# Performance work log

Hardware: AMD Instinct MI355X
Metric: run time of the kernel (lower is better)

## Reference

```python
import jax, jax.numpy as jnp
import numpy as np

B, INP, OUP = 16, 64, 64
T, H, W = 30, 64, 44
KD, KH, KW = 3, 3, 3
M, G = 2, 2
INP_GAP = max(16, INP // 16)          # 16
GROUPS = G * OUP                       # 128 (wn_fc2 groups)
IN_PG = (M * OUP) // GROUPS            # 1  in-channels per group
OUT_PG = (OUP * INP * KD * KH * KW) // GROUPS  # 864 out-channels per group


def setup_inputs() -> dict:
    key = jax.random.key(0)
    ks = jax.random.split(key, 6)
    x = jax.random.normal(ks[0], (B, INP, T, H, W), dtype=jnp.float32)
    # reduce: 1x1x1 conv INP -> INP_GAP (with bias), acts on [B, INP, 1,1,1]
    w_reduce = jax.random.normal(ks[1], (INP_GAP, INP), dtype=jnp.float32) * 0.05
    b_reduce = jax.random.normal(ks[2], (INP_GAP,), dtype=jnp.float32) * 0.05
    # wn_fc1: 1x1x1 conv INP_GAP -> M*OUP (with bias)
    w_fc1 = jax.random.normal(ks[3], (M * OUP, INP_GAP), dtype=jnp.float32) * 0.05
    b_fc1 = jax.random.normal(ks[4], (M * OUP,), dtype=jnp.float32) * 0.05
    # wn_fc2: grouped 1x1x1 conv, no bias: [groups, out_per_group, in_per_group]
    w_fc2 = jax.random.normal(ks[5], (GROUPS, OUT_PG, IN_PG), dtype=jnp.float32) * 0.02
    return {"x": x, "w_reduce": w_reduce, "b_reduce": b_reduce,
            "w_fc1": w_fc1, "b_fc1": b_fc1, "w_fc2": w_fc2}


def reference(x, w_reduce, b_reduce, w_fc1, b_fc1, w_fc2):
    # Global average pool over T,H,W -> [B, INP]; 1x1x1 convs are matmuls.
    x_gap = x.mean(axis=(2, 3, 4))                       # [B, INP]
    g = x_gap @ w_reduce.T + b_reduce                     # [B, INP_GAP]
    h = jax.nn.sigmoid(g @ w_fc1.T + b_fc1)               # [B, M*OUP]
    # Grouped 1x1 conv (groups=GROUPS): group-major channel layout matches
    # torch's conv output ordering, so a plain reshape reproduces .view().
    hg = h.reshape(B, GROUPS, IN_PG)                      # [B, G*OUP, 1]
    wdyn = jnp.einsum('goi,bgi->bgo', w_fc2, hg)          # [B, GROUPS, OUT_PG]
    wdyn = wdyn.reshape(B, OUP, INP, KD, KH, KW)          # per-sample conv weights

    # Per-sample conv3d (groups=1), stride 1, padding 1 on D,H,W.
    def conv_one(xi, wi):
        # xi: [INP, T, H, W], wi: [OUP, INP, KD, KH, KW]
        return jax.lax.conv_general_dilated(
            xi[None], wi, window_strides=(1, 1, 1),
            padding=[(1, 1), (1, 1), (1, 1)],
            dimension_numbers=('NCDHW', 'OIDHW', 'NCDHW'))[0]

    return jax.vmap(conv_one)(x, wdyn)                    # [B, OUP, T, H, W]
```

## Files before the change

kernel.cpp:

```cpp
#include <hip/hip_runtime.h>
#include <hip/hip_bf16.h>
#include <stdint.h>

#define B_ 16
#define T_ 30
#define H_ 64
#define W_ 44
#define HW_ (H_*W_)
#define THW_ (T_*HW_)

#define HP_ 66
#define WP_ 46
#define PPLANE_ (HP_*WP_)
#define PPOS_ (T_*PPLANE_)

#define SZ2 4
#define SY2 10
#define SX2 18
#define NS2 (SZ2*SY2*SX2)

#define SWZ(v) (((v) >> 1) & 3)

typedef __bf16 bf16x8 __attribute__((ext_vector_type(8)));
typedef float f32x4 __attribute__((ext_vector_type(4)));

static __device__ __forceinline__ short f2bf(float f) {
    __hip_bfloat16 h = __float2bfloat16(f);
    union { __hip_bfloat16 b; short s; } u; u.b = h; return u.s;
}

static __device__ __forceinline__ void gload_lds16(const short* g, short* l) {
    __builtin_amdgcn_global_load_lds((const __attribute__((address_space(1))) void*)g,
                                     (__attribute__((address_space(3))) void*)l, 16, 0, 0);
}

__global__ __launch_bounds__(256) void transpose_kernel(const float* __restrict__ x,
                                                        short* __restrict__ xt,
                                                        float* __restrict__ gap) {
    __shared__ short lb[64*52];
    __shared__ float gsum[64];
    int blk = blockIdx.x;
    int b = blk / (T_*HP_);
    int r = blk - b*(T_*HP_);
    int t = r / HP_;
    int hp = r - t*HP_;
    int tid = threadIdx.x;
    bool interior = (hp >= 1) && (hp <= H_);
    float rsum = 0.f;
    {
        int ic = tid >> 2, g = tid & 3;
        if (interior) {
            int h = hp - 1;
            const float4* row = (const float4*)(x + ((size_t)(b*64 + ic)*T_ + t)*HW_ + h*W_);
            #pragma unroll
            for (int q = g; q < 11; q += 4) {
                float4 v = row[q];
                short4 s4;
                s4.x = f2bf(v.x); s4.y = f2bf(v.y); s4.z = f2bf(v.z); s4.w = f2bf(v.w);
                *(short4*)&lb[ic*52 + q*4] = s4;
                rsum += (v.x + v.y) + (v.z + v.w);
            }
        }
        rsum += __shfl_xor(rsum, 1);
        rsum += __shfl_xor(rsum, 2);
        if ((tid & 3) == 0) gsum[ic] = rsum;
    }
    __syncthreads();
    if (interior && tid < 64)
        atomicAdd(&gap[b*64 + tid], gsum[tid] * (1.0f / THW_));
    for (int e = tid; e < WP_*16; e += 256) {
        int wp = e >> 4, i4 = (e & 15) * 4;
        short4 s4 = make_short4(0,0,0,0);
        if (interior && wp >= 1 && wp <= W_) {
            int w = wp - 1;
            s4.x = lb[(i4+0)*52 + w];
            s4.y = lb[(i4+1)*52 + w];
            s4.z = lb[(i4+2)*52 + w];
            s4.w = lb[(i4+3)*52 + w];
        }
        size_t pos = (size_t)t*PPLANE_ + hp*WP_ + wp;
        short* dst = xt + ((size_t)(b*2 + (i4 >> 5))*PPOS_ + pos)*32 + (i4 & 31);
        *(short4*)dst = s4;
    }
}

__global__ __launch_bounds__(256) void fc_kernel(const float* __restrict__ gap,
        const float* __restrict__ w_reduce, const float* __restrict__ b_reduce,
        const float* __restrict__ w_fc1, const float* __restrict__ b_fc1,
        float* __restrict__ h_out) {
    __shared__ float gl[256];
    int t = threadIdx.x;
    {
        int b = t >> 4, j = t & 15;
        float a = b_reduce[j];
        #pragma unroll
        for (int c = 0; c < 64; ++c) a += gap[b*64 + c] * w_reduce[j*64 + c];
        gl[b*16 + j] = a;
    }
    __syncthreads();
    for (int idx = t; idx < 2048; idx += 256) {
        int b = idx >> 7, j = idx & 127;
        float v = b_fc1[j];
        #pragma unroll
        for (int i = 0; i < 16; ++i) v += gl[b*16 + i] * w_fc1[j*16 + i];
        h_out[idx] = 1.0f / (1.0f + expf(-v));
    }
}

__global__ __launch_bounds__(256) void wdyn_kernel(const float* __restrict__ w_fc2,
        const float* __restrict__ h, short* __restrict__ wdyn, short* __restrict__ zblk) {
    if (blockIdx.x == 0 && threadIdx.x < 128) zblk[threadIdx.x] = 0;
    int b = blockIdx.x / 27, tap = blockIdx.x % 27;
    short* dst = wdyn + ((size_t)b*27 + tap) * 4096;
    for (int e = threadIdx.x; e < 4096; e += 256) {
        int oc = e >> 6, ic = e & 63;
        float wv = w_fc2[(oc*64 + ic)*27 + tap];
        float hv = h[b*128 + 2*oc + (ic >> 5)];
        dst[e] = f2bf(wv * hv);
    }
}

#define DO_STEP(tap, r0, r1, r2, r3) do {                              \
    int _kd = (tap)/9, _rr = (tap)-_kd*9, _kh = _rr/3, _kw = _rr-_kh*3;\
    int _sb = (tzw + _kd)*180 + (hw4 + _kh)*18 + _kw + ln;             \
    __builtin_amdgcn_s_setprio(1);                                     \
    _Pragma("unroll")                                                  \
    for (int _j = 0; _j < 4; ++_j) {                                   \
        int _s = _sb + _j*18;                                          \
        bf16x8 _bv = *(const bf16x8*)&xs[_s*32 + ((kg ^ SWZ(_s)) * 8)];\
        acc[0][_j] = __builtin_amdgcn_mfma_f32_16x16x32_bf16(r0, _bv, acc[0][_j], 0, 0, 0); \
        acc[1][_j] = __builtin_amdgcn_mfma_f32_16x16x32_bf16(r1, _bv, acc[1][_j], 0, 0, 0); \
        acc[2][_j] = __builtin_amdgcn_mfma_f32_16x16x32_bf16(r2, _bv, acc[2][_j], 0, 0, 0); \
        acc[3][_j] = __builtin_amdgcn_mfma_f32_16x16x32_bf16(r3, _bv, acc[3][_j], 0, 0, 0); \
    }                                                                  \
    __builtin_amdgcn_s_setprio(0);                                     \
} while (0)

__global__ __launch_bounds__(256, 3) void conv_kernel(const short* __restrict__ xt,
        const short* __restrict__ wdyn, const short* __restrict__ zblk,
        float* __restrict__ out) {
    __shared__ short xs[NS2*32];
    __shared__ short wb[2048];

    int bid = (blockIdx.x & 7) * 720 + (blockIdx.x >> 3);
    int b = bid / 360; int r = bid - b*360;
    int tzt = r / 24; r -= tzt*24;
    int tyt = r / 3;  int txt = r - tyt*3;
    int t0 = tzt*2, h0 = tyt*8, w0 = txt*16;

    int tid = threadIdx.x, wid = tid >> 6, lane = tid & 63;
    int ln = lane & 15, kg = lane >> 4;
    int l4 = lane >> 2, c = lane & 3;
    int tzw = wid & 1, hw4 = (wid >> 1) * 4;
    int woc = tid >> 2, wseg = tid & 3;

    const short* wdb = wdyn + (size_t)b * 27 * 4096;

    f32x4 acc[4][4];
    #pragma unroll
    for (int mt = 0; mt < 4; ++mt)
        #pragma unroll
        for (int j = 0; j < 4; ++j) acc[mt][j] = f32x4{0.f, 0.f, 0.f, 0.f};

    auto stage_x = [&](int half) {
        const short* xbh = xt + (size_t)(b*2 + half) * PPOS_ * 32;
        #pragma unroll
        for (int ii = 0; ii < 12; ++ii) {
            int inst = ii*4 + wid;
            if (inst < 45) {
                int s = inst*16 + l4;
                int z = s / 180; int rr = s - z*180;
                int y = rr / 18; int xx = rr - y*18;
                int t = t0 + z - 1;
                int seg = (c ^ SWZ(s)) * 8;
                const short* src = ((unsigned)t < (unsigned)T_)
                    ? xbh + ((size_t)t*PPLANE_ + (h0+y)*WP_ + (w0+xx))*32 + seg
                    : zblk + seg;
                gload_lds16(src, xs + inst*512);
            }
        }
    };

    stage_x(0);
    uint4 wr = *(const uint4*)(wdb + woc*64 + wseg*8);
    short* wdst = wb + woc*32 + ((wseg ^ SWZ(woc)) * 8);

    for (int g = 0; g < 54; ++g) {
        __syncthreads();
        *(uint4*)wdst = wr;
        if (g < 53) {
            int gn = g + 1;
            int nt = gn - ((gn >= 27) ? 27 : 0);
            int nh = (gn >= 27) ? 32 : 0;
            wr = *(const uint4*)(wdb + nt*4096 + nh + woc*64 + wseg*8);
        }
        __syncthreads();
        bf16x8 a0, a1, a2, a3;
        {
            int cw = (kg ^ SWZ(ln)) * 8;
            a0 = *(const bf16x8*)&wb[(ln     )*32 + cw];
            a1 = *(const bf16x8*)&wb[(ln + 16)*32 + cw];
            a2 = *(const bf16x8*)&wb[(ln + 32)*32 + cw];
            a3 = *(const bf16x8*)&wb[(ln + 48)*32 + cw];
        }
        int tap = g - ((g >= 27) ? 27 : 0);
        DO_STEP(tap, a0, a1, a2, a3);
        if (g == 26) {
            __syncthreads();
            stage_x(1);
        }
    }

    int t = t0 + tzw;
    int wv = w0 + ln;
    if (wv < W_) {
        #pragma unroll
        for (int mt = 0; mt < 4; ++mt) {
            size_t obase = ((size_t)(b*64 + mt*16 + kg*4) * T_ + t) * HW_;
            #pragma unroll
            for (int j = 0; j < 4; ++j) {
                float* o = out + obase + (h0 + hw4 + j)*W_ + wv;
                #pragma unroll
                for (int ri = 0; ri < 4; ++ri)
                    o[(size_t)ri * THW_] = acc[mt][j][ri];
            }
        }
    }
}

extern "C" void kernel_launch(void* const* d_in, const int* in_sizes, int n_in,
                              void* d_out, int out_size, void* d_ws, size_t ws_size,
                              hipStream_t stream) {
    const float* x        = (const float*)d_in[0];
    const float* w_reduce = (const float*)d_in[1];
    const float* b_reduce = (const float*)d_in[2];
    const float* w_fc1    = (const float*)d_in[3];
    const float* b_fc1    = (const float*)d_in[4];
    const float* w_fc2    = (const float*)d_in[5];
    float* out = (float*)d_out;

    float* gap  = (float*)d_ws;
    float* h    = gap + 1024;
    short* wdyn = (short*)(h + 2048);
    short* zblk = wdyn + (size_t)B_*27*4096;
    short* xt   = zblk + 128;

    hipMemsetAsync(gap, 0, 1024*sizeof(float), stream);
    transpose_kernel<<<B_*T_*HP_, 256, 0, stream>>>(x, xt, gap);
    fc_kernel       <<<1,         256, 0, stream>>>(gap, w_reduce, b_reduce, w_fc1, b_fc1, h);
    wdyn_kernel     <<<B_*27,     256, 0, stream>>>(w_fc2, h, wdyn, zblk);
    conv_kernel     <<<B_*360,    256, 0, stream>>>(xt, wdyn, zblk, out);
}
```

Before: 530.3 us.

## Double-buffer dynamic weight tiles in LDS with one barrier per tap

Turns the per-tap weight staging buffer into two LDS buffers. The next tap's weights are written while the current tap's MFMAs read the other buffer, and global loads are prefetched two steps ahead. This lets each of the 54 steps use a single barrier instead of two, and the tap loop is fully unrolled. The cost is an extra 4 KB of LDS per block and hand-written s_waitcnt/s_barrier sequences whose correctness depends on precise wait counts, plus larger code from unrolling.

```diff
diff --git a/kernel.cpp b/kernel.cpp
--- a/kernel.cpp
+++ b/kernel.cpp
@@ -136,11 +136,33 @@
     __builtin_amdgcn_s_setprio(0);                                     \
 } while (0)
 
+#define FULLSTEP(g) do {                                               \
+    if ((g) < 53) {                                                    \
+        *(uint4*)(wbb + ((((g)+1)&1) ? 2048 : 0) + woff) = wr;         \
+        if ((g) <= 51) wr = wload((g)+2);                              \
+    }                                                                  \
+    bf16x8 a0, a1, a2, a3;                                             \
+    {                                                                  \
+        const short* _wq = wbb + (((g)&1) ? 2048 : 0);                 \
+        int _cw = (kg ^ SWZ(ln)) * 8;                                  \
+        a0 = *(const bf16x8*)&_wq[(ln     )*32 + _cw];                 \
+        a1 = *(const bf16x8*)&_wq[(ln + 16)*32 + _cw];                 \
+        a2 = *(const bf16x8*)&_wq[(ln + 32)*32 + _cw];                 \
+        a3 = *(const bf16x8*)&_wq[(ln + 48)*32 + _cw];                 \
+    }                                                                  \
+    DO_STEP((g) - (((g) >= 27) ? 27 : 0), a0, a1, a2, a3);             \
+} while (0)
+
+#define STEP_SYNC() do {                                               \
+    asm volatile("s_waitcnt lgkmcnt(0)" ::: "memory");                 \
+    __builtin_amdgcn_s_barrier();                                      \
+} while (0)
+
 __global__ __launch_bounds__(256, 3) void conv_kernel(const short* __restrict__ xt,
         const short* __restrict__ wdyn, const short* __restrict__ zblk,
         float* __restrict__ out) {
     __shared__ short xs[NS2*32];
-    __shared__ short wb[2048];
+    __shared__ short wb[2][2048];
 
     int bid = (blockIdx.x & 7) * 720 + (blockIdx.x >> 3);
     int b = bid / 360; int r = bid - b*360;
@@ -153,6 +175,8 @@
     int l4 = lane >> 2, c = lane & 3;
     int tzw = wid & 1, hw4 = (wid >> 1) * 4;
     int woc = tid >> 2, wseg = tid & 3;
+    int woff = woc*32 + ((wseg ^ SWZ(woc)) * 8);
+    short* wbb = &wb[0][0];
 
     const short* wdb = wdyn + (size_t)b * 27 * 4096;
 
@@ -162,6 +186,11 @@
         #pragma unroll
         for (int j = 0; j < 4; ++j) acc[mt][j] = f32x4{0.f, 0.f, 0.f, 0.f};
 
+    auto wload = [&](int gn) {
+        int tap = gn - ((gn >= 27) ? 27 : 0);
+        int nh  = (gn >= 27) ? 32 : 0;
+        return *(const uint4*)(wdb + tap*4096 + nh + woc*64 + wseg*8);
+    };
     auto stage_x = [&](int half) {
         const short* xbh = xt + (size_t)(b*2 + half) * PPOS_ * 32;
         #pragma unroll
@@ -182,32 +211,22 @@
     };
 
     stage_x(0);
-    uint4 wr = *(const uint4*)(wdb + woc*64 + wseg*8);
-    short* wdst = wb + woc*32 + ((wseg ^ SWZ(woc)) * 8);
-
+    uint4 wr = wload(0);
+    asm volatile("s_waitcnt vmcnt(0)" ::: "memory");
+    *(uint4*)(wbb + woff) = wr;
+    wr = wload(1);
+    STEP_SYNC();
+
+    #pragma unroll
     for (int g = 0; g < 54; ++g) {
-        __syncthreads();
-        *(uint4*)wdst = wr;
-        if (g < 53) {
-            int gn = g + 1;
-            int nt = gn - ((gn >= 27) ? 27 : 0);
-            int nh = (gn >= 27) ? 32 : 0;
-            wr = *(const uint4*)(wdb + nt*4096 + nh + woc*64 + wseg*8);
-        }
-        __syncthreads();
-        bf16x8 a0, a1, a2, a3;
-        {
-            int cw = (kg ^ SWZ(ln)) * 8;
-            a0 = *(const bf16x8*)&wb[(ln     )*32 + cw];
-            a1 = *(const bf16x8*)&wb[(ln + 16)*32 + cw];
-            a2 = *(const bf16x8*)&wb[(ln + 32)*32 + cw];
-            a3 = *(const bf16x8*)&wb[(ln + 48)*32 + cw];
-        }
-        int tap = g - ((g >= 27) ? 27 : 0);
-        DO_STEP(tap, a0, a1, a2, a3);
+        FULLSTEP(g);
         if (g == 26) {
-            __syncthreads();
+            STEP_SYNC();
             stage_x(1);
+            asm volatile("s_waitcnt vmcnt(0)" ::: "memory");
+            __builtin_amdgcn_s_barrier();
+        } else if (g < 53) {
+            STEP_SYNC();
         }
     }
 
```

Measured after the change: 803.6 us. 51.5% more time.
